# Kernel optimization log

Hardware: AMD Instinct MI355X
Metric: run time of the kernel (lower is better)

The kernel has to match this reference:

```python
import jax, jax.numpy as jnp
import numpy as np
from jax import lax

B, C, D, H, W = 2, 64, 20, 20, 20


def _conv3d(x, w, b, pad):
    # x: [B,C,D,H,W], w: [O,I,kd,kh,kw]
    y = lax.conv_general_dilated(
        x, w, window_strides=(1, 1, 1), padding=pad,
        dimension_numbers=('NCDHW', 'OIDHW', 'NCDHW'))
    return y + b[None, :, None, None, None]


def setup_inputs() -> dict:
    key = jax.random.key(0)
    ks = jax.random.split(key, 7)
    s = 1.0 / np.sqrt(C * 3)  # conv fan-in = C*1*3*1
    return {
        'x': jax.random.normal(ks[0], (B, C, D, H, W), jnp.float32),
        'q_w': jax.random.uniform(ks[1], (C, C, 1, 3, 1), jnp.float32, -s, s),
        'q_b': jax.random.uniform(ks[2], (C,), jnp.float32, -s, s),
        'k_w': jax.random.uniform(ks[3], (C, C, 3, 1, 1), jnp.float32, -s, s),
        'k_b': jax.random.uniform(ks[4], (C,), jnp.float32, -s, s),
        'v_w': jax.random.uniform(ks[5], (C, C, 1, 1, 3), jnp.float32, -s, s),
        'v_b': jax.random.uniform(ks[6], (C,), jnp.float32, -s, s),
    }


def reference(x, q_w, q_b, k_w, k_b, v_w, v_b):
    b, c, d, h, w = x.shape
    n = d * h * w
    q0 = _conv3d(x, q_w, q_b, ((0, 0), (1, 1), (0, 0))).reshape(b, c, n)
    k0 = _conv3d(x, k_w, k_b, ((1, 1), (0, 0), (0, 0))).reshape(b, c, n)
    v = _conv3d(x, v_w, v_b, ((0, 0), (0, 0), (1, 1))).reshape(b, c, n)
    # scores[b, i, j] = sum_c k0[b,c,i] * q0[b,c,j]  -> [B, N, N]
    scores = jnp.einsum('bci,bcj->bij', k0, q0)
    # torch Softmax(dim=1) on [B,N,N] normalizes over axis 1 (the i axis)
    attn = jax.nn.softmax(scores, axis=1)
    out = jnp.einsum('bcn,bnm->bcm', v, attn)  # v @ attn
    return out.reshape(b, c, d, h, w)
```

## Files before the change

### kernel.cpp

```cpp
#include <hip/hip_runtime.h>
#include <cstdint>
#include <cstddef>

typedef _Float16 half4_t  __attribute__((ext_vector_type(4)));
typedef _Float16 half8_t  __attribute__((ext_vector_type(8)));
typedef short    short4_t __attribute__((ext_vector_type(4)));
typedef unsigned short ushort4_t __attribute__((ext_vector_type(4)));
typedef float    f32x4_t  __attribute__((ext_vector_type(4)));

#define LOG2E 1.44269504088896340736f

__device__ __forceinline__ float bf2f(unsigned short u) {
    union { unsigned int u; float f; } x;
    x.u = ((unsigned int)u) << 16;
    return x.f;
}
__device__ __forceinline__ unsigned short f2bf(float f) {
    union { float f; unsigned int u; } x;
    x.f = f;
    unsigned int r = (x.u + 0x7FFFu + ((x.u >> 16) & 1u)) >> 16;
    return (unsigned short)r;
}
__device__ __forceinline__ unsigned short f2bf_fast(float f) {
    union { float f; unsigned int u; } x;
    x.f = f;
    return (unsigned short)((x.u + 0x8000u) >> 16);
}

__global__ __launch_bounds__(256) void prep_kernel(
    const void* __restrict__ x,
    const void* __restrict__ qw, const void* __restrict__ kw, const void* __restrict__ vw,
    const void* __restrict__ qb, const void* __restrict__ kb, const void* __restrict__ vb,
    int* __restrict__ flag,
    _Float16* __restrict__ w2, float* __restrict__ bb, _Float16* __restrict__ xT)
{
    __shared__ int scnt;
    __shared__ _Float16 tile[64][66];

    if (threadIdx.x == 0) scnt = 0;
    __syncthreads();
    {
        unsigned int w = ((const unsigned int*)x)[threadIdx.x];
        int e = (w >> 7) & 0xFF;
        int hit = (e == 0) || (e >= 0x68 && e <= 0x88);
        atomicAdd(&scnt, hit);
    }
    __syncthreads();
    const int bf = (scnt >= 128) ? 1 : 0;
    if (blockIdx.x == 0 && threadIdx.x == 0) flag[0] = bf;

    if (blockIdx.x < 144) {
        int idx = blockIdx.x * 256 + threadIdx.x;
        if (idx < 36864) {
            int conv = idx / 12288;
            int r    = idx - conv * 12288;
            int tap  = r >> 12;
            int r2   = r & 4095;
            int co   = r2 >> 6;
            int ci   = r2 & 63;
            const void* w = (conv == 0) ? qw : (conv == 1) ? kw : vw;
            float t;
            if (bf) t = bf2f(((const unsigned short*)w)[co * 192 + ci * 3 + tap]);
            else    t = ((const float*)w)[co * 192 + ci * 3 + tap];
            if (conv == 0) t *= LOG2E;
            w2[idx] = (_Float16)t;
        }
        if (idx < 192) {
            int a = idx >> 6, co = idx & 63;
            const void* s = (a == 0) ? qb : (a == 1) ? kb : vb;
            float t = bf ? bf2f(((const unsigned short*)s)[co]) : ((const float*)s)[co];
            if (a == 0) t *= LOG2E;
            bb[idx] = t;
        }
    } else {
        const int bx   = blockIdx.x - 144;
        const int b    = bx / 125;
        const int n0   = (bx - b * 125) * 64;
        const int lane = threadIdx.x & 63;
        const int wv   = threadIdx.x >> 6;

        if (bf) {
            const unsigned short* xb = (const unsigned short*)x + (size_t)b * 512000 + n0 + lane;
#pragma unroll
            for (int i = 0; i < 16; ++i) {
                const int ci = wv * 16 + i;
                tile[ci][lane] = (_Float16)bf2f(xb[(size_t)ci * 8000]);
            }
        } else {
            const float* xb = (const float*)x + (size_t)b * 512000 + n0 + lane;
#pragma unroll
            for (int i = 0; i < 16; ++i) {
                const int ci = wv * 16 + i;
                tile[ci][lane] = (_Float16)xb[(size_t)ci * 8000];
            }
        }
        __syncthreads();
        _Float16* out = xT + ((size_t)b * 8000 + n0) * 64 + lane;
#pragma unroll
        for (int i = 0; i < 16; ++i) {
            const int r = wv * 16 + i;
            out[(size_t)r * 64] = tile[lane][r];
        }
    }
}

__global__ __launch_bounds__(256, 2) void convg_kernel(
    const _Float16* __restrict__ xT, const _Float16* __restrict__ w2,
    const float* __restrict__ bb,
    _Float16* __restrict__ Qt, _Float16* __restrict__ Kt, unsigned short* __restrict__ Vt)
{
    const int tid = threadIdx.x;
    const int wv  = tid >> 6;
    const int L   = tid & 63;
    const int q4  = L >> 4;
    const int lm  = L & 15;
    const int W    = blockIdx.x * 4 + wv;
    const int conv = W % 3;
    const int u    = W / 3;
    const int b    = u / 250;
    const int n0   = (u - b * 250) * 32;

    half8_t wf[3][2][4];
    const _Float16* wbase = w2 + (size_t)conv * 12288;
#pragma unroll
    for (int tap = 0; tap < 3; ++tap)
#pragma unroll
        for (int kh = 0; kh < 2; ++kh)
#pragma unroll
            for (int cb = 0; cb < 4; ++cb)
                wf[tap][kh][cb] = *(const half8_t*)(
                    wbase + ((size_t)(tap * 64 + cb * 16 + lm)) * 64 + kh * 32 + q4 * 8);

    f32x4_t acc[2][4];
#pragma unroll
    for (int cb = 0; cb < 4; ++cb) {
        const float bi = bb[conv * 64 + cb * 16 + lm];
        const f32x4_t v = (f32x4_t){bi, bi, bi, bi};
        acc[0][cb] = v;
        acc[1][cb] = v;
    }

    const _Float16* xb = xT + (size_t)b * 512000;
    const half8_t z8 = {(_Float16)0, (_Float16)0, (_Float16)0, (_Float16)0,
                        (_Float16)0, (_Float16)0, (_Float16)0, (_Float16)0};

#pragma unroll
    for (int mt = 0; mt < 2; ++mt) {
        const int npos = n0 + mt * 16 + lm;
        int gm, gp, off;
        if (conv == 0)      { const int h = (npos / 20) % 20; gm = h > 0; gp = h < 19; off = 20; }
        else if (conv == 1) { const int d = npos / 400;       gm = d > 0; gp = d < 19; off = 400; }
        else                { const int w = npos % 20;        gm = w > 0; gp = w < 19; off = 1; }
        const int rm = gm ? npos - off : npos;
        const int rp = gp ? npos + off : npos;

#pragma unroll
        for (int kh = 0; kh < 2; ++kh) {
            const int ko = kh * 32 + q4 * 8;
            half8_t a0 = *(const half8_t*)(xb + (size_t)rm * 64 + ko);
            const half8_t a1 = *(const half8_t*)(xb + (size_t)npos * 64 + ko);
            half8_t a2 = *(const half8_t*)(xb + (size_t)rp * 64 + ko);
            a0 = gm ? a0 : z8;
            a2 = gp ? a2 : z8;
#pragma unroll
            for (int cb = 0; cb < 4; ++cb) {
                acc[mt][cb] = __builtin_amdgcn_mfma_f32_16x16x32_f16(a0, wf[0][kh][cb], acc[mt][cb], 0, 0, 0);
                acc[mt][cb] = __builtin_amdgcn_mfma_f32_16x16x32_f16(a1, wf[1][kh][cb], acc[mt][cb], 0, 0, 0);
                acc[mt][cb] = __builtin_amdgcn_mfma_f32_16x16x32_f16(a2, wf[2][kh][cb], acc[mt][cb], 0, 0, 0);
            }
        }
    }

    if (conv < 2) {
        _Float16* dst = (conv == 0) ? Qt : Kt;
#pragma unroll
        for (int mt = 0; mt < 2; ++mt)
#pragma unroll
            for (int cb = 0; cb < 4; ++cb)
#pragma unroll
                for (int reg = 0; reg < 4; ++reg) {
                    const int n = n0 + mt * 16 + q4 * 4 + reg;
                    dst[((size_t)b * 8000 + n) * 64 + cb * 16 + lm] = (_Float16)acc[mt][cb][reg];
                }
    } else {
#pragma unroll
        for (int mt = 0; mt < 2; ++mt)
#pragma unroll
            for (int cb = 0; cb < 4; ++cb) {
                ushort4_t vvv;
#pragma unroll
                for (int reg = 0; reg < 4; ++reg) vvv[reg] = f2bf(acc[mt][cb][reg]);
                *(ushort4_t*)(Vt + ((size_t)b * 64 + cb * 16 + lm) * 8000 + n0 + mt * 16 + q4 * 4) = vvv;
            }
    }
}

__global__ __launch_bounds__(256, 2) void attn_kernel(
    const _Float16* __restrict__ Qt, const _Float16* __restrict__ Kt,
    const unsigned short* __restrict__ Vt,
    _Float16* __restrict__ Oseg, float* __restrict__ Wseg)
{
    __shared__ __align__(16) _Float16       k_lds[2][4096];
    __shared__ __align__(16) unsigned short v_lds[2][4096];

    const int tid = threadIdx.x;
    const int wv  = tid >> 6;
    const int L   = tid & 63;
    const int q4  = L >> 4;
    const int lm  = L & 15;
    const int qt  = blockIdx.x;
    const int b   = blockIdx.y;
    const int sp  = blockIdx.z;
    const int NS  = gridDim.z;
    const int t0  = (125 * sp) / NS;
    const int t1  = (125 * (sp + 1)) / NS;
    const int unit = qt * 4 + wv;

    const _Float16* Qb = Qt + ((size_t)b * 8000 + (size_t)qt * 128 + wv * 32 + lm) * 64 + q4 * 8;
    half8_t bq00 = *(const half8_t*)(Qb);
    half8_t bq01 = *(const half8_t*)(Qb + 32);
    half8_t bq10 = *(const half8_t*)(Qb + 16 * 64);
    half8_t bq11 = *(const half8_t*)(Qb + 16 * 64 + 32);

    f32x4_t o[2][4];
    f32x4_t acc_l[2];
#pragma unroll
    for (int mt = 0; mt < 2; ++mt) {
        acc_l[mt] = (f32x4_t){0.f, 0.f, 0.f, 0.f};
#pragma unroll
        for (int cb = 0; cb < 4; ++cb) o[mt][cb] = (f32x4_t){0.f, 0.f, 0.f, 0.f};
    }
    const short4_t ones4 = {(short)0x3F80, (short)0x3F80, (short)0x3F80, (short)0x3F80};

    const _Float16*       Kg = Kt + (size_t)b * 512000;
    const unsigned short* Vg = Vt + (size_t)b * 512000;
    const int r0  = tid >> 3;
    const int cc0 = tid & 7;
    const int swz_lo = r0 * 64 + ((cc0 ^ (r0 & 7)) * 8);
    const int swz_hi = (r0 + 32) * 64 + ((cc0 ^ (r0 & 7)) * 8);
    const _Float16*       Kr0 = Kg + (size_t)r0 * 64 + cc0 * 8;
    const _Float16*       Kr1 = Kg + (size_t)(r0 + 32) * 64 + cc0 * 8;
    const unsigned short* Vr0 = Vg + (size_t)r0 * 8000 + cc0 * 8;
    const unsigned short* Vr1 = Vg + (size_t)(r0 + 32) * 8000 + cc0 * 8;

    uint4 sk0, sk1, sv0, sv1;

    {
        const int n0 = t0 * 64;
        sk0 = *(const uint4*)(Kr0 + (size_t)n0 * 64);
        sk1 = *(const uint4*)(Kr1 + (size_t)n0 * 64);
        sv0 = *(const uint4*)(Vr0 + n0);
        sv1 = *(const uint4*)(Vr1 + n0);
        *(uint4*)(&k_lds[0][swz_lo]) = sk0;
        *(uint4*)(&k_lds[0][swz_hi]) = sk1;
        *(uint4*)(&v_lds[0][swz_lo]) = sv0;
        *(uint4*)(&v_lds[0][swz_hi]) = sv1;
        if (t0 + 1 < t1) {
            const int n1 = (t0 + 1) * 64;
            sk0 = *(const uint4*)(Kr0 + (size_t)n1 * 64);
            sk1 = *(const uint4*)(Kr1 + (size_t)n1 * 64);
            sv0 = *(const uint4*)(Vr0 + n1);
            sv1 = *(const uint4*)(Vr1 + n1);
        }
    }

    int p = 0;
    for (int kt = t0; kt < t1; ++kt) {
        __syncthreads();
        if (kt + 1 < t1) {
            *(uint4*)(&k_lds[p ^ 1][swz_lo]) = sk0;
            *(uint4*)(&k_lds[p ^ 1][swz_hi]) = sk1;
            *(uint4*)(&v_lds[p ^ 1][swz_lo]) = sv0;
            *(uint4*)(&v_lds[p ^ 1][swz_hi]) = sv1;
            if (kt + 2 < t1) {
                const int n2 = (kt + 2) * 64;
                sk0 = *(const uint4*)(Kr0 + (size_t)n2 * 64);
                sk1 = *(const uint4*)(Kr1 + (size_t)n2 * 64);
                sv0 = *(const uint4*)(Vr0 + n2);
                sv1 = *(const uint4*)(Vr1 + n2);
            }
        }

        short4_t pfr[2][4];
#pragma unroll
        for (int ns = 0; ns < 4; ++ns) {
            const int n = ns * 16 + lm;
            const _Float16* krow = &k_lds[p][n * 64];
            const half8_t ak0 = *(const half8_t*)(krow + (((q4    ) ^ (n & 7)) * 8));
            const half8_t ak1 = *(const half8_t*)(krow + (((q4 + 4) ^ (n & 7)) * 8));
#pragma unroll
            for (int mt = 0; mt < 2; ++mt) {
                f32x4_t z = (f32x4_t){0.f, 0.f, 0.f, 0.f};
                z = __builtin_amdgcn_mfma_f32_16x16x32_f16(ak0, mt ? bq10 : bq00, z, 0, 0, 0);
                z = __builtin_amdgcn_mfma_f32_16x16x32_f16(ak1, mt ? bq11 : bq01, z, 0, 0, 0);
                short4_t pk;
#pragma unroll
                for (int reg = 0; reg < 4; ++reg)
                    pk[reg] = (short)f2bf_fast(exp2f(z[reg]));
                pfr[mt][ns] = pk;
            }
        }

#pragma unroll
        for (int mt = 0; mt < 2; ++mt)
#pragma unroll
            for (int ns = 0; ns < 4; ++ns)
                acc_l[mt] = __builtin_amdgcn_mfma_f32_16x16x16bf16_1k(ones4, pfr[mt][ns], acc_l[mt], 0, 0, 0);

#pragma unroll
        for (int cb = 0; cb < 4; ++cb) {
            const int c = cb * 16 + lm;
            const unsigned short* vrow = &v_lds[p][c * 64];
            f32x4_t a0 = o[0][cb], a1 = o[1][cb];
#pragma unroll
            for (int ns = 0; ns < 4; ++ns) {
                const int cc = ns * 2 + (q4 >> 1);
                const short4_t av = *(const short4_t*)(vrow + ((cc ^ (c & 7)) * 8) + (q4 & 1) * 4);
                a0 = __builtin_amdgcn_mfma_f32_16x16x16bf16_1k(av, pfr[0][ns], a0, 0, 0, 0);
                a1 = __builtin_amdgcn_mfma_f32_16x16x16bf16_1k(av, pfr[1][ns], a1, 0, 0, 0);
            }
            o[0][cb] = a0;
            o[1][cb] = a1;
        }
        p ^= 1;
    }

    if (unit >= 250) return;

    float rinv[2], lg[2];
#pragma unroll
    for (int mt = 0; mt < 2; ++mt) {
        const float l = acc_l[mt][0];
        rinv[mt] = 1.0f / l;
        lg[mt]   = __log2f(l);
    }

    const int seg = (b * 250 + unit) * NS + sp;
    _Float16* os = Oseg + (size_t)seg * 2048;
#pragma unroll
    for (int mt = 0; mt < 2; ++mt) {
#pragma unroll
        for (int cb = 0; cb < 4; ++cb) {
            half4_t e;
#pragma unroll
            for (int reg = 0; reg < 4; ++reg) e[reg] = (_Float16)(o[mt][cb][reg] * rinv[mt]);
            *(half4_t*)(os + (mt * 16 + lm) * 64 + cb * 16 + q4 * 4) = e;
        }
    }
    if (q4 == 0) {
#pragma unroll
        for (int mt = 0; mt < 2; ++mt)
            Wseg[(size_t)seg * 32 + mt * 16 + lm] = lg[mt];
    }
}

__global__ __launch_bounds__(256, 2) void combine_kernel(
    const _Float16* __restrict__ Oseg, const float* __restrict__ Wseg,
    const int* __restrict__ flag, void* __restrict__ outv, int NS)
{
    __shared__ float wls[8 * 32];
    __shared__ float cls[8 * 32];
    const int tid = threadIdx.x;
    const int qt = blockIdx.x, b = blockIdx.y;
    const int base = (b * 250 + qt) * NS;

    for (int i = tid; i < NS * 32; i += 256) wls[i] = Wseg[(size_t)base * 32 + i];
    __syncthreads();
    if (tid < 32) {
        const int r = tid;
        float wm = wls[r];
        for (int s2 = 1; s2 < NS; ++s2) wm = fmaxf(wm, wls[s2 * 32 + r]);
        float cs = 0.f;
        for (int s2 = 0; s2 < NS; ++s2) {
            float cc = exp2f(wls[s2 * 32 + r] - wm);
            cls[s2 * 32 + r] = cc;
            cs += cc;
        }
        const float inv = 1.f / cs;
        for (int s2 = 0; s2 < NS; ++s2) cls[s2 * 32 + r] *= inv;
    }
    __syncthreads();

    const int c = tid & 63, rg = tid >> 6;
    float acc[8];
#pragma unroll
    for (int i = 0; i < 8; ++i) acc[i] = 0.f;
    for (int s2 = 0; s2 < NS; ++s2) {
        const _Float16* src = Oseg + ((size_t)(base + s2)) * 2048 + rg * 8 * 64 + c;
        const float* cf = &cls[s2 * 32 + rg * 8];
#pragma unroll
        for (int i = 0; i < 8; ++i) acc[i] += (float)src[i * 64] * cf[i];
    }

    const size_t ob = ((size_t)b * 64 + c) * 8000 + qt * 32 + rg * 8;
    if (*flag) {
        uint4 u0;
        u0.x = f2bf(acc[0]) | ((unsigned)f2bf(acc[1]) << 16);
        u0.y = f2bf(acc[2]) | ((unsigned)f2bf(acc[3]) << 16);
        u0.z = f2bf(acc[4]) | ((unsigned)f2bf(acc[5]) << 16);
        u0.w = f2bf(acc[6]) | ((unsigned)f2bf(acc[7]) << 16);
        *(uint4*)((unsigned short*)outv + ob) = u0;
    } else {
        float* o32 = (float*)outv + ob;
        *(f32x4_t*)(o32)     = (f32x4_t){acc[0], acc[1], acc[2], acc[3]};
        *(f32x4_t*)(o32 + 4) = (f32x4_t){acc[4], acc[5], acc[6], acc[7]};
    }
}

extern "C" void kernel_launch(void* const* d_in, const int* in_sizes, int n_in,
                              void* d_out, int out_size, void* d_ws, size_t ws_size,
                              hipStream_t stream)
{
    (void)in_sizes; (void)n_in; (void)out_size;
    const void* x  = d_in[0];
    const void* qw = d_in[1];
    const void* qb = d_in[2];
    const void* kw = d_in[3];
    const void* kb = d_in[4];
    const void* vw = d_in[5];
    const void* vb = d_in[6];

    char* ws = (char*)d_ws;
    int*            flag = (int*)ws;
    float*          bb   = (float*)(ws + 2304);
    _Float16*       w2   = (_Float16*)(ws + 3072);
    _Float16*       Qt   = (_Float16*)(ws + 76800);
    _Float16*       Kt   = (_Float16*)(ws + 2124800);
    unsigned short* Vt   = (unsigned short*)(ws + 4172800);
    _Float16*       xT   = (_Float16*)(ws + 6220800);

    const size_t need8 = 23116800;
    const int NS = (ws_size >= need8) ? 8 : 1;
    _Float16* Oseg = (_Float16*)(ws + 6220800);
    float*    Wseg = (float*)(ws + 6220800 + (size_t)2 * 250 * NS * 2048 * 2);

    prep_kernel<<<dim3(394), 256, 0, stream>>>(x, qw, kw, vw, qb, kb, vb, flag, w2, bb, xT);
    convg_kernel<<<dim3(375), 256, 0, stream>>>(xT, w2, bb, Qt, Kt, Vt);
    attn_kernel<<<dim3(63, 2, NS), 256, 0, stream>>>(Qt, Kt, Vt, Oseg, Wseg);
    combine_kernel<<<dim3(250, 2), 256, 0, stream>>>(Oseg, Wseg, flag, d_out, NS);
}
```

Baseline: 152.1 us.

## Halve per-wave query tile to 16 rows and double attention grid

Each wave now handles 16 query columns instead of 32, so the attention grid grows from 63 to 125 blocks per batch/split and the combine kernel from 250 to 500 blocks. This removes the padded tail units and raises parallelism and occupancy through lower register pressure. In exchange, each K/V tile loaded into LDS is reused by half as many MFMAs, so global and LDS traffic per unit of compute doubles.

Measured after the change: 156.8 us. +3.1%, slower.

```diff
diff --git a/kernel.cpp b/kernel.cpp
--- a/kernel.cpp
+++ b/kernel.cpp
@@ -214,22 +214,16 @@
     const int NS  = gridDim.z;
     const int t0  = (125 * sp) / NS;
     const int t1  = (125 * (sp + 1)) / NS;
-    const int unit = qt * 4 + wv;
-
-    const _Float16* Qb = Qt + ((size_t)b * 8000 + (size_t)qt * 128 + wv * 32 + lm) * 64 + q4 * 8;
-    half8_t bq00 = *(const half8_t*)(Qb);
-    half8_t bq01 = *(const half8_t*)(Qb + 32);
-    half8_t bq10 = *(const half8_t*)(Qb + 16 * 64);
-    half8_t bq11 = *(const half8_t*)(Qb + 16 * 64 + 32);
-
-    f32x4_t o[2][4];
-    f32x4_t acc_l[2];
-#pragma unroll
-    for (int mt = 0; mt < 2; ++mt) {
-        acc_l[mt] = (f32x4_t){0.f, 0.f, 0.f, 0.f};
-#pragma unroll
-        for (int cb = 0; cb < 4; ++cb) o[mt][cb] = (f32x4_t){0.f, 0.f, 0.f, 0.f};
-    }
+    const int u   = qt * 4 + wv;
+
+    const _Float16* Qb = Qt + ((size_t)b * 8000 + (size_t)qt * 64 + wv * 16 + lm) * 64 + q4 * 8;
+    half8_t bq0 = *(const half8_t*)(Qb);
+    half8_t bq1 = *(const half8_t*)(Qb + 32);
+
+    f32x4_t o[4];
+    f32x4_t acc_l = (f32x4_t){0.f, 0.f, 0.f, 0.f};
+#pragma unroll
+    for (int cb = 0; cb < 4; ++cb) o[cb] = (f32x4_t){0.f, 0.f, 0.f, 0.f};
     const short4_t ones4 = {(short)0x3F80, (short)0x3F80, (short)0x3F80, (short)0x3F80};
 
     const _Float16*       Kg = Kt + (size_t)b * 512000;
@@ -281,129 +275,106 @@
             }
         }
 
-        short4_t pfr[2][4];
+        short4_t pfr[4];
 #pragma unroll
         for (int ns = 0; ns < 4; ++ns) {
             const int n = ns * 16 + lm;
             const _Float16* krow = &k_lds[p][n * 64];
             const half8_t ak0 = *(const half8_t*)(krow + (((q4    ) ^ (n & 7)) * 8));
             const half8_t ak1 = *(const half8_t*)(krow + (((q4 + 4) ^ (n & 7)) * 8));
-#pragma unroll
-            for (int mt = 0; mt < 2; ++mt) {
-                f32x4_t z = (f32x4_t){0.f, 0.f, 0.f, 0.f};
-                z = __builtin_amdgcn_mfma_f32_16x16x32_f16(ak0, mt ? bq10 : bq00, z, 0, 0, 0);
-                z = __builtin_amdgcn_mfma_f32_16x16x32_f16(ak1, mt ? bq11 : bq01, z, 0, 0, 0);
-                short4_t pk;
-#pragma unroll
-                for (int reg = 0; reg < 4; ++reg)
-                    pk[reg] = (short)f2bf_fast(exp2f(z[reg]));
-                pfr[mt][ns] = pk;
-            }
-        }
-
-#pragma unroll
-        for (int mt = 0; mt < 2; ++mt)
-#pragma unroll
-            for (int ns = 0; ns < 4; ++ns)
-                acc_l[mt] = __builtin_amdgcn_mfma_f32_16x16x16bf16_1k(ones4, pfr[mt][ns], acc_l[mt], 0, 0, 0);
+            f32x4_t z = (f32x4_t){0.f, 0.f, 0.f, 0.f};
+            z = __builtin_amdgcn_mfma_f32_16x16x32_f16(ak0, bq0, z, 0, 0, 0);
+            z = __builtin_amdgcn_mfma_f32_16x16x32_f16(ak1, bq1, z, 0, 0, 0);
+            short4_t pk;
+#pragma unroll
+            for (int reg = 0; reg < 4; ++reg)
+                pk[reg] = (short)f2bf_fast(exp2f(z[reg]));
+            pfr[ns] = pk;
+        }
+
+#pragma unroll
+        for (int ns = 0; ns < 4; ++ns)
+            acc_l = __builtin_amdgcn_mfma_f32_16x16x16bf16_1k(ones4, pfr[ns], acc_l, 0, 0, 0);
 
 #pragma unroll
         for (int cb = 0; cb < 4; ++cb) {
             const int c = cb * 16 + lm;
             const unsigned short* vrow = &v_lds[p][c * 64];
-            f32x4_t a0 = o[0][cb], a1 = o[1][cb];
+            f32x4_t a0 = o[cb];
 #pragma unroll
             for (int ns = 0; ns < 4; ++ns) {
                 const int cc = ns * 2 + (q4 >> 1);
                 const short4_t av = *(const short4_t*)(vrow + ((cc ^ (c & 7)) * 8) + (q4 & 1) * 4);
-                a0 = __builtin_amdgcn_mfma_f32_16x16x16bf16_1k(av, pfr[0][ns], a0, 0, 0, 0);
-                a1 = __builtin_amdgcn_mfma_f32_16x16x16bf16_1k(av, pfr[1][ns], a1, 0, 0, 0);
-            }
-            o[0][cb] = a0;
-            o[1][cb] = a1;
+                a0 = __builtin_amdgcn_mfma_f32_16x16x16bf16_1k(av, pfr[ns], a0, 0, 0, 0);
+            }
+            o[cb] = a0;
         }
         p ^= 1;
     }
 
-    if (unit >= 250) return;
-
-    float rinv[2], lg[2];
-#pragma unroll
-    for (int mt = 0; mt < 2; ++mt) {
-        const float l = acc_l[mt][0];
-        rinv[mt] = 1.0f / l;
-        lg[mt]   = __log2f(l);
-    }
-
-    const int seg = (b * 250 + unit) * NS + sp;
-    _Float16* os = Oseg + (size_t)seg * 2048;
-#pragma unroll
-    for (int mt = 0; mt < 2; ++mt) {
-#pragma unroll
-        for (int cb = 0; cb < 4; ++cb) {
-            half4_t e;
-#pragma unroll
-            for (int reg = 0; reg < 4; ++reg) e[reg] = (_Float16)(o[mt][cb][reg] * rinv[mt]);
-            *(half4_t*)(os + (mt * 16 + lm) * 64 + cb * 16 + q4 * 4) = e;
-        }
-    }
-    if (q4 == 0) {
-#pragma unroll
-        for (int mt = 0; mt < 2; ++mt)
-            Wseg[(size_t)seg * 32 + mt * 16 + lm] = lg[mt];
-    }
+    const float l = acc_l[0];
+    const float rinv = 1.0f / l;
+    const float lg   = __log2f(l);
+
+    const int seg = (b * 500 + u) * NS + sp;
+    _Float16* os = Oseg + (size_t)seg * 1024;
+#pragma unroll
+    for (int cb = 0; cb < 4; ++cb) {
+        half4_t e;
+#pragma unroll
+        for (int reg = 0; reg < 4; ++reg) e[reg] = (_Float16)(o[cb][reg] * rinv);
+        *(half4_t*)(os + lm * 64 + cb * 16 + q4 * 4) = e;
+    }
+    if (q4 == 0) Wseg[(size_t)seg * 16 + lm] = lg;
 }
 
 __global__ __launch_bounds__(256, 2) void combine_kernel(
     const _Float16* __restrict__ Oseg, const float* __restrict__ Wseg,
     const int* __restrict__ flag, void* __restrict__ outv, int NS)
 {
-    __shared__ float wls[8 * 32];
-    __shared__ float cls[8 * 32];
+    __shared__ float wls[8 * 16];
+    __shared__ float cls[8 * 16];
     const int tid = threadIdx.x;
-    const int qt = blockIdx.x, b = blockIdx.y;
-    const int base = (b * 250 + qt) * NS;
-
-    for (int i = tid; i < NS * 32; i += 256) wls[i] = Wseg[(size_t)base * 32 + i];
+    const int u = blockIdx.x, b = blockIdx.y;
+    const int base = (b * 500 + u) * NS;
+
+    for (int i = tid; i < NS * 16; i += 256) wls[i] = Wseg[(size_t)base * 16 + i];
     __syncthreads();
-    if (tid < 32) {
+    if (tid < 16) {
         const int r = tid;
         float wm = wls[r];
-        for (int s2 = 1; s2 < NS; ++s2) wm = fmaxf(wm, wls[s2 * 32 + r]);
+        for (int s2 = 1; s2 < NS; ++s2) wm = fmaxf(wm, wls[s2 * 16 + r]);
         float cs = 0.f;
         for (int s2 = 0; s2 < NS; ++s2) {
-            float cc = exp2f(wls[s2 * 32 + r] - wm);
-            cls[s2 * 32 + r] = cc;
+            float cc = exp2f(wls[s2 * 16 + r] - wm);
+            cls[s2 * 16 + r] = cc;
             cs += cc;
         }
         const float inv = 1.f / cs;
-        for (int s2 = 0; s2 < NS; ++s2) cls[s2 * 32 + r] *= inv;
+        for (int s2 = 0; s2 < NS; ++s2) cls[s2 * 16 + r] *= inv;
     }
     __syncthreads();
 
     const int c = tid & 63, rg = tid >> 6;
-    float acc[8];
-#pragma unroll
-    for (int i = 0; i < 8; ++i) acc[i] = 0.f;
+    float acc[4];
+#pragma unroll
+    for (int i = 0; i < 4; ++i) acc[i] = 0.f;
     for (int s2 = 0; s2 < NS; ++s2) {
-        const _Float16* src = Oseg + ((size_t)(base + s2)) * 2048 + rg * 8 * 64 + c;
-        const float* cf = &cls[s2 * 32 + rg * 8];
-#pragma unroll
-        for (int i = 0; i < 8; ++i) acc[i] += (float)src[i * 64] * cf[i];
-    }
-
-    const size_t ob = ((size_t)b * 64 + c) * 8000 + qt * 32 + rg * 8;
+        const _Float16* src = Oseg + ((size_t)(base + s2)) * 1024 + rg * 4 * 64 + c;
+        const float* cf = &cls[s2 * 16 + rg * 4];
+#pragma unroll
+        for (int i = 0; i < 4; ++i) acc[i] += (float)src[i * 64] * cf[i];
+    }
+
+    const size_t ob = ((size_t)b * 64 + c) * 8000 + u * 16 + rg * 4;
     if (*flag) {
-        uint4 u0;
+        uint2 u0;
         u0.x = f2bf(acc[0]) | ((unsigned)f2bf(acc[1]) << 16);
         u0.y = f2bf(acc[2]) | ((unsigned)f2bf(acc[3]) << 16);
-        u0.z = f2bf(acc[4]) | ((unsigned)f2bf(acc[5]) << 16);
-        u0.w = f2bf(acc[6]) | ((unsigned)f2bf(acc[7]) << 16);
-        *(uint4*)((unsigned short*)outv + ob) = u0;
+        *(uint2*)((unsigned short*)outv + ob) = u0;
     } else {
         float* o32 = (float*)outv + ob;
-        *(f32x4_t*)(o32)     = (f32x4_t){acc[0], acc[1], acc[2], acc[3]};
-        *(f32x4_t*)(o32 + 4) = (f32x4_t){acc[4], acc[5], acc[6], acc[7]};
+        *(f32x4_t*)(o32) = (f32x4_t){acc[0], acc[1], acc[2], acc[3]};
     }
 }
 
@@ -432,10 +403,10 @@
     const size_t need8 = 23116800;
     const int NS = (ws_size >= need8) ? 8 : 1;
     _Float16* Oseg = (_Float16*)(ws + 6220800);
-    float*    Wseg = (float*)(ws + 6220800 + (size_t)2 * 250 * NS * 2048 * 2);
+    float*    Wseg = (float*)(ws + 6220800 + (size_t)2 * 500 * NS * 1024 * 2);
 
     prep_kernel<<<dim3(394), 256, 0, stream>>>(x, qw, kw, vw, qb, kb, vb, flag, w2, bb, xT);
     convg_kernel<<<dim3(375), 256, 0, stream>>>(xT, w2, bb, Qt, Kt, Vt);
-    attn_kernel<<<dim3(63, 2, NS), 256, 0, stream>>>(Qt, Kt, Vt, Oseg, Wseg);
-    combine_kernel<<<dim3(250, 2), 256, 0, stream>>>(Oseg, Wseg, flag, d_out, NS);
-}
+    attn_kernel<<<dim3(125, 2, NS), 256, 0, stream>>>(Qt, Kt, Vt, Oseg, Wseg);
+    combine_kernel<<<dim3(500, 2), 256, 0, stream>>>(Oseg, Wseg, flag, d_out, NS);
+}
```
